# Kernel optimization log

Measured on AMD Instinct MI355X. Metric: run time of the kernel, lower is better.

## Reference

```python
import jax, jax.numpy as jnp
import numpy as np

INF = 1.0e12
V, EMB, H, H2 = 50000, 300, 512, 1024
EDGE, EEMB = 4, 32
B, TS, TQ = 16, 400, 33
MAX_OOV = 100
EXT = V + MAX_OOV
COV_HYPER = 1.0


def gru_cell(x, h, Wi, Wh, bi, bh):
    # torch GRU cell, gate order r,z,n
    gx = x @ Wi.T + bi
    gh = h @ Wh.T + bh
    hd = h.shape[-1]
    r = jax.nn.sigmoid(gx[:, :hd] + gh[:, :hd])
    z = jax.nn.sigmoid(gx[:, hd:2 * hd] + gh[:, hd:2 * hd])
    n = jnp.tanh(gx[:, 2 * hd:] + r * gh[:, 2 * hd:])
    return (1.0 - z) * n + z * h


def gru_scan(xs, h0, Wi, Wh, bi, bh, reverse=False):
    def step(h, x):
        hn = gru_cell(x, h, Wi, Wh, bi, bh)
        return hn, hn
    return jax.lax.scan(step, h0, xs, reverse=reverse)


def setup_inputs() -> dict:
    key = jax.random.key(0)
    ks = iter(jax.random.split(key, 64))
    def rp(*shape):
        return jax.random.normal(next(ks), shape, jnp.float32) * 0.05
    d = {}
    d['enc_emb'] = rp(V, EMB); d['ans_emb'] = rp(EDGE, EEMB); d['dec_emb'] = rp(V, EMB)
    in0 = EMB + EEMB
    d['eWi0'] = rp(2, 3 * H, in0); d['eWh0'] = rp(2, 3 * H, H); d['ebi0'] = rp(2, 3 * H); d['ebh0'] = rp(2, 3 * H)
    d['eWi1'] = rp(2, 3 * H, 2 * H); d['eWh1'] = rp(2, 3 * H, H); d['ebi1'] = rp(2, 3 * H); d['ebh1'] = rp(2, 3 * H)
    d['trans_W'] = rp(H2, H2); d['trans_b'] = rp(H2)
    d['upd_W'] = rp(H2, 2 * H2); d['gate_W'] = rp(H2, 2 * H2)
    din0 = EMB + H2
    d['dWi0'] = rp(3 * H2, din0); d['dWh0'] = rp(3 * H2, H2); d['dbi0'] = rp(3 * H2); d['dbh0'] = rp(3 * H2)
    d['dWi1'] = rp(3 * H2, H2); d['dWh1'] = rp(3 * H2, H2); d['dbi1'] = rp(3 * H2); d['dbh1'] = rp(3 * H2)
    d['dtrans_W'] = rp(H2, H2); d['dtrans_b'] = rp(H2)
    d['pW1'] = rp(H2, 2 * H2); d['pb1'] = rp(H2); d['pW2'] = rp(V, H2); d['pb2'] = rp(V)
    d['input_s'] = jax.random.randint(next(ks), (B, TS), 1, V)
    ext = jax.random.randint(next(ks), (B, TS), 0, EXT)
    d['ext_src_ids'] = ext.at[0, 0].set(EXT - 1)  # pin num_oov = MAX_OOV
    d['input_q'] = jax.random.randint(next(ks), (B, TQ), 1, V)
    d['input_a'] = jax.random.randint(next(ks), (B, TS), 0, EDGE)
    d['s_pos'] = jax.random.randint(next(ks), (B, TS), 0, TS)
    return d


def reference(enc_emb, ans_emb, dec_emb,
              eWi0, eWh0, ebi0, ebh0, eWi1, eWh1, ebi1, ebh1,
              trans_W, trans_b, upd_W, gate_W,
              dWi0, dWh0, dbi0, dbh0, dWi1, dWh1, dbi1, dbh1,
              dtrans_W, dtrans_b, pW1, pb1, pW2, pb2,
              input_s, ext_src_ids, input_q, input_a, s_pos):
    mask = jnp.sign(input_s)  # [B,TS] (all ones by construction)
    # ---------------- encoder ----------------
    emb = jnp.concatenate([enc_emb[input_s], ans_emb[input_a]], -1)  # [B,TS,EMB+EEMB]
    xs = emb.transpose(1, 0, 2)  # [TS,B,*]
    h0 = jnp.zeros((B, H), emb.dtype)
    h_list = []
    for (Wi, Wh, bi, bh) in ((eWi0, eWh0, ebi0, ebh0), (eWi1, eWh1, ebi1, ebh1)):
        hf, yf = gru_scan(xs, h0, Wi[0], Wh[0], bi[0], bh[0])
        hb, yb = gru_scan(xs, h0, Wi[1], Wh[1], bi[1], bh[1], reverse=True)
        xs = jnp.concatenate([yf, yb], -1)
        h_list.append(jnp.concatenate([hf, hb], -1))  # [B,H2]
    output = xs.transpose(1, 0, 2)  # [B,TS,H2]
    memories = output @ trans_W.T + trans_b
    # gated self-attention
    energies = jnp.einsum('btd,bsd->bts', output, memories)
    energies = jnp.where(mask[:, None, :] == 0, -INF, energies)
    scores = jax.nn.softmax(energies, -1)
    ctx = jnp.einsum('bts,bsd->btd', scores, output)
    inp = jnp.concatenate([output, ctx], -1)
    f_t = jnp.tanh(inp @ upd_W.T)
    g_t = jax.nn.sigmoid(inp @ gate_W.T)
    self_out = g_t * f_t + (1.0 - g_t) * output
    # answer-sentence attention (on memories, per original code)
    ans = jnp.where(input_a[..., None] == 0, 1.0, memories)
    e = memories * ans
    e = jnp.where(mask[..., None] == 0, -INF, e)
    e = jax.nn.softmax(e, axis=1)
    enc_out = self_out + e * memories
    # ---------------- decoder ----------------
    mem_d = enc_out @ dtrans_W.T + dtrans_b  # [B,TS,H2]
    emb_q = dec_emb[input_q[:, :-1]].transpose(1, 0, 2)  # [Tt,B,EMB]
    b_idx = jnp.arange(B)[:, None]

    def step(carry, emb_t):
        h0c, h1c, ctx_c, cov = carry
        rnn_in = jnp.concatenate([emb_t, ctx_c], -1)
        h0n = gru_cell(rnn_in, h0c, dWi0, dWh0, dbi0, dbh0)
        h1n = gru_cell(h0n, h1c, dWi1, dWh1, dbi1, dbh1)
        energy = jnp.einsum('bd,btd->bt', h1n, mem_d)
        sen_e = jnp.where(mask == 0, -INF, energy)
        cov_e = sen_e * (1.0 - cov)
        attn = jax.nn.softmax(cov_e, -1)
        new_ctx = jnp.einsum('bt,btd->bd', attn, mem_d)
        cov_loss = jnp.sum(jnp.minimum(attn, cov)) / B * COV_HYPER
        new_cov = cov + attn
        hid = jnp.tanh(jnp.concatenate([h1n, new_ctx], -1) @ pW1.T + pb1)
        logits = hid @ pW2.T + pb2
        ext = jnp.concatenate([logits, jnp.zeros((B, MAX_OOV), logits.dtype)], -1)
        out = jnp.full((B, EXT), -INF, logits.dtype).at[b_idx, ext_src_ids].max(cov_e)
        out = jnp.where(out == -INF, 0.0, out)
        lg = ext + out
        lg = jnp.where(lg == 0.0, -INF, lg)
        return (h0n, h1n, new_ctx, new_cov), (lg, cov_loss)

    init = (h_list[0], h_list[1], jnp.zeros((B, H2), emb.dtype), jnp.zeros((B, TS), emb.dtype))
    _, (lgs, covl) = jax.lax.scan(step, init, emb_q)
    return lgs.transpose(1, 0, 2), jnp.sum(covl) / lgs.shape[0]


if __name__ == '__main__':
    o = reference(**setup_inputs())
    print(o[0].shape, o[1])
```

## Files before the change

### kernel.cpp

```cpp
#include <hip/hip_runtime.h>
#include <stdint.h>

#define TSN 400
#define NB 16
#define HENC 512
#define HD2 1024
#define G3E 1536
#define G3D 3072
#define EMBD 300
#define AEMB 32
#define NV 50000
#define NEXT 50100
#define NVP 50176
#define NTT 32
#define NEG_INF (-1.0e12f)

typedef __attribute__((ext_vector_type(8))) short bf16x8;
typedef __attribute__((ext_vector_type(4))) float f32x4;

__device__ __forceinline__ ushort f2bf(float f) {
  unsigned u = __float_as_uint(f);
  unsigned r = (u + 0x7fffu + ((u >> 16) & 1u)) >> 16;
  return (ushort)r;
}
__device__ __forceinline__ float bf2f(ushort h) {
  return __uint_as_float((unsigned)h << 16);
}
__device__ __forceinline__ unsigned agat_ld(const unsigned* p) {
  return __hip_atomic_load(p, __ATOMIC_RELAXED, __HIP_MEMORY_SCOPE_AGENT);
}
__device__ __forceinline__ void agat_st(unsigned* p, unsigned v) {
  __hip_atomic_store(p, v, __ATOMIC_RELAXED, __HIP_MEMORY_SCOPE_AGENT);
}
__device__ __forceinline__ unsigned long long agat_ld64(const unsigned long long* p) {
  return __hip_atomic_load(p, __ATOMIC_RELAXED, __HIP_MEMORY_SCOPE_AGENT);
}

__global__ __launch_bounds__(256) void k_embed_bf(
    const float* __restrict__ enc_emb, const float* __restrict__ ans_emb,
    const int* __restrict__ input_s, const int* __restrict__ input_a,
    ushort* __restrict__ X0)
{
  long i = (long)blockIdx.x*256 + threadIdx.x;
  if (i >= (long)TSN*NB*384) return;
  int c = (int)(i % 384);
  long r = i / 384;
  int b = (int)(r % NB);
  int t = (int)(r / NB);
  float v = 0.f;
  if (c < EMBD) v = enc_emb[(long)input_s[b*TSN + t]*EMBD + c];
  else if (c < 332) v = ans_emb[(long)input_a[b*TSN + t]*AEMB + (c - EMBD)];
  X0[i] = f2bf(v);
}

__global__ __launch_bounds__(256) void k_embq_bf(
    const float* __restrict__ dec_emb, const int* __restrict__ input_q,
    ushort* __restrict__ EQ)
{
  long i = (long)blockIdx.x*256 + threadIdx.x;
  if (i >= (long)NTT*NB*320) return;
  int c = (int)(i % 320);
  long r = i / 320;
  int b = (int)(r % NB);
  int s = (int)(r / NB);
  EQ[i] = (c < EMBD) ? f2bf(dec_emb[(long)input_q[b*33 + s]*EMBD + c]) : (ushort)0;
}

__global__ __launch_bounds__(256) void k_castw(
    const float* __restrict__ src, ushort* __restrict__ dst,
    int Nsrc, long total, int Ksrc, int Kdst, int ldsrc, int coloff)
{
  long i = (long)blockIdx.x*256 + threadIdx.x;
  if (i >= total) return;
  int k = (int)(i % Kdst);
  long n = i / Kdst;
  float v = (n < Nsrc && k < Ksrc) ? src[n*ldsrc + coloff + k] : 0.f;
  dst[i] = f2bf(v);
}

__global__ __launch_bounds__(256) void k_cast8(
    const float4* __restrict__ s, ushort* __restrict__ d, long n8)
{
  long i = (long)blockIdx.x*256 + threadIdx.x;
  if (i >= n8) return;
  float4 v0 = s[2*i], v1 = s[2*i + 1];
  union { ushort u[8]; bf16x8 h; } c;
  c.u[0] = f2bf(v0.x); c.u[1] = f2bf(v0.y); c.u[2] = f2bf(v0.z); c.u[3] = f2bf(v0.w);
  c.u[4] = f2bf(v1.x); c.u[5] = f2bf(v1.y); c.u[6] = f2bf(v1.z); c.u[7] = f2bf(v1.w);
  *(bf16x8*)&d[i*8] = c.h;
}

__global__ __launch_bounds__(256) void k_cast(
    const float* __restrict__ s, ushort* __restrict__ d, long n)
{
  long i = (long)blockIdx.x*256 + threadIdx.x;
  if (i >= n) return;
  d[i] = f2bf(s[i]);
}

__global__ __launch_bounds__(256) void k_catcopy(
    const unsigned* __restrict__ src, unsigned* __restrict__ dst)
{
  long i = (long)blockIdx.x*256 + threadIdx.x;
  if (i >= 6400l*512) return;
  long r = i >> 9;
  int c = (int)(i & 511);
  dst[(r << 10) + c] = src[i];
}

__global__ __launch_bounds__(256) void k_transpose_hh(
    const ushort* __restrict__ in, ushort* __restrict__ out)
{
  __shared__ ushort tb[32][33];
  int b = blockIdx.z;
  int r0 = blockIdx.x*32, c0 = blockIdx.y*32;
  int tx = threadIdx.x & 31, ty = threadIdx.x >> 5;
  #pragma unroll
  for (int i = 0; i < 32; i += 8) {
    int r = r0 + ty + i, c = c0 + tx;
    tb[ty+i][tx] = (r < TSN) ? in[((long)b*TSN + r)*1024 + c] : (ushort)0;
  }
  __syncthreads();
  #pragma unroll
  for (int i = 0; i < 32; i += 8) {
    int c = c0 + ty + i, r = r0 + tx;
    out[((long)b*1024 + c)*448 + r] = tb[tx][ty+i];
  }
}

__global__ __launch_bounds__(256) void k_mfma_nt(
    const ushort* __restrict__ Ab, const ushort* __restrict__ Wb,
    const float* __restrict__ bias, float* __restrict__ Cb, ushort* __restrict__ C2b,
    int M, int N, int K, int lda, int ldw, int ldc,
    long sA, long sW, long sC, long sBias, int accum, int act)
{
  __shared__ ushort As[64][72];
  __shared__ ushort Ws[64][72];
  const ushort* A = Ab + (long)blockIdx.z * sA;
  const ushort* W = Wb + (long)blockIdx.z * sW;
  float* C = Cb ? Cb + (long)blockIdx.z * sC : nullptr;
  const float* bi = bias ? bias + (long)blockIdx.z * sBias : nullptr;
  const int m0 = blockIdx.x*64, n0 = blockIdx.y*64;
  const int tid = threadIdx.x;
  const int wave = tid >> 6, lane = tid & 63;
  const int wm = wave >> 1, wn = wave & 1;
  const int lr = lane & 15, kg = lane >> 4;
  f32x4 acc[2][2] = {};
  for (int k0 = 0; k0 < K; k0 += 64) {
    __syncthreads();
    #pragma unroll
    for (int it = 0; it < 2; ++it) {
      int sidx = tid + it*256;
      int r = sidx >> 3, c = (sidx & 7)*8;
      bf16x8 av = {};
      bf16x8 wv = {};
      if (m0 + r < M) av = *(const bf16x8*)&A[(long)(m0+r)*lda + k0 + c];
      if (n0 + r < N) wv = *(const bf16x8*)&W[(long)(n0+r)*ldw + k0 + c];
      *(bf16x8*)&As[r][c] = av;
      *(bf16x8*)&Ws[r][c] = wv;
    }
    __syncthreads();
    #pragma unroll
    for (int kk = 0; kk < 2; ++kk) {
      bf16x8 af[2], bf[2];
      #pragma unroll
      for (int mt = 0; mt < 2; ++mt)
        af[mt] = *(const bf16x8*)&As[wm*32 + mt*16 + lr][kk*32 + kg*8];
      #pragma unroll
      for (int nt = 0; nt < 2; ++nt)
        bf[nt] = *(const bf16x8*)&Ws[wn*32 + nt*16 + lr][kk*32 + kg*8];
      #pragma unroll
      for (int mt = 0; mt < 2; ++mt)
        #pragma unroll
        for (int nt = 0; nt < 2; ++nt)
          acc[mt][nt] = __builtin_amdgcn_mfma_f32_16x16x32_bf16(af[mt], bf[nt], acc[mt][nt], 0, 0, 0);
    }
  }
  #pragma unroll
  for (int mt = 0; mt < 2; ++mt) {
    #pragma unroll
    for (int r = 0; r < 4; ++r) {
      int m = m0 + wm*32 + mt*16 + kg*4 + r;
      if (m >= M) continue;
      #pragma unroll
      for (int nt = 0; nt < 2; ++nt) {
        int n = n0 + wn*32 + nt*16 + lr;
        if (n >= N) continue;
        float v = acc[mt][nt][r];
        if (accum && C) v += C[(long)m*ldc + n];
        if (bi)    v += bi[n];
        if (act == 1) v = tanhf(v);
        else if (act == 2) v = 1.f/(1.f + expf(-v));
        if (C) C[(long)m*ldc + n] = v;
        if (C2b) C2b[(long)blockIdx.z*sC + (long)m*ldc + n] = f2bf(v);
      }
    }
  }
}

__global__ __launch_bounds__(256, 1) void k_scan_mfma(
    const ushort* __restrict__ GXf, const ushort* __restrict__ GXb,
    const ushort* __restrict__ Whb,
    const float* __restrict__ bh,
    ushort* __restrict__ Ybf, int bmajor,
    float* __restrict__ hfin,
    ushort* __restrict__ hpp,
    int* __restrict__ slots)
{
  const int bid = blockIdx.x;
  const int tid = threadIdx.x;
  const int wg = bid*4 + (tid >> 6);
  const int lane = tid & 63;
  const int lr = lane & 15, kg = lane >> 4;
  const int dir = wg >> 5, jt = wg & 31;
  const int j = jt*16 + lr;
  __shared__ ushort hsm[16][520];
  const ushort* Wp0 = Whb + ((long)(dir*G3E + j)        << 9) + kg*8;
  const ushort* Wp1 = Whb + ((long)(dir*G3E + 512 + j)  << 9) + kg*8;
  const ushort* Wp2 = Whb + ((long)(dir*G3E + 1024 + j) << 9) + kg*8;
  bf16x8 W0[16], W1[16], W2[16];
  #pragma unroll
  for (int i = 0; i < 16; ++i) {
    W0[i] = *(const bf16x8*)(Wp0 + i*32);
    W1[i] = *(const bf16x8*)(Wp1 + i*32);
    W2[i] = *(const bf16x8*)(Wp2 + i*32);
  }
  const float bh0 = bh[dir*G3E + j];
  const float bh1 = bh[dir*G3E + 512 + j];
  const float bh2 = bh[dir*G3E + 1024 + j];
  const ushort* GX = dir ? GXb : GXf;
  unsigned* hppu = (unsigned*)hpp;
  int* myslot = slots + dir*256 + (bid & 7)*32;
  int* dslots = slots + dir*256;
  float hreg[4] = {0.f, 0.f, 0.f, 0.f};
  float g0[4], g1[4], g2[4];
  {
    const int t0 = dir ? (TSN - 1) : 0;
    const ushort* gxp = GX + (long)t0*NB*G3E + j;
    #pragma unroll
    for (int r = 0; r < 4; ++r) {
      const ushort* g = gxp + (long)(kg*4 + r)*G3E;
      g0[r] = bf2f(g[0]); g1[r] = bf2f(g[512]); g2[r] = bf2f(g[1024]);
    }
  }
  for (int s = 0; s < TSN; ++s) {
    const int cur = s & 1;
    {
      const unsigned long long* hin =
          (const unsigned long long*)hppu + (cur*2 + dir)*2048;
      unsigned long long vqw[8];
      #pragma unroll
      for (int i = 0; i < 8; ++i) vqw[i] = agat_ld64(hin + i*256 + tid);
      #pragma unroll
      for (int i = 0; i < 8; ++i) {
        int d0 = 2*(i*256 + tid);
        *(unsigned long long*)&hsm[d0 >> 8][(d0 & 255)*2] = vqw[i];
      }
    }
    __syncthreads();
    f32x4 a0 = {}, a1 = {}, a2 = {};
    #pragma unroll
    for (int i = 0; i < 16; ++i) {
      bf16x8 hf = *(const bf16x8*)&hsm[lr][kg*8 + i*32];
      a0 = __builtin_amdgcn_mfma_f32_16x16x32_bf16(hf, W0[i], a0, 0, 0, 0);
      a1 = __builtin_amdgcn_mfma_f32_16x16x32_bf16(hf, W1[i], a1, 0, 0, 0);
      a2 = __builtin_amdgcn_mfma_f32_16x16x32_bf16(hf, W2[i], a2, 0, 0, 0);
    }
    const int t = dir ? (TSN - 1 - s) : s;
    const int obase = ((cur^1)*2 + dir)*16*512;
    float hsave[4];
    #pragma unroll
    for (int r = 0; r < 4; ++r) {
      int b = kg*4 + r;
      float rr = 1.f/(1.f + expf(-(g0[r] + a0[r] + bh0)));
      float zz = 1.f/(1.f + expf(-(g1[r] + a1[r] + bh1)));
      float nn = tanhf(g2[r] + rr*(a2[r] + bh2));
      float hn = (1.f - zz)*nn + zz*hreg[r];
      hreg[r] = hn;
      hsave[r] = hn;
      unsigned hv = f2bf(hn);
      unsigned pv = (unsigned)__shfl_xor((int)hv, 1);
      if ((lr & 1) == 0)
        agat_st(hppu + ((obase + b*512 + j) >> 1), hv | (pv << 16));
    }
    if (s + 1 < TSN) {
      asm volatile("s_waitcnt vmcnt(0)" ::: "memory");
      __syncthreads();
      if (tid == 0)
        agat_st((unsigned*)myslot, (unsigned)(s + 1));
      {
        const int tn = dir ? (TSN - 2 - s) : (s + 1);
        const ushort* gxp = GX + (long)tn*NB*G3E + j;
        #pragma unroll
        for (int r = 0; r < 4; ++r) {
          const ushort* g = gxp + (long)(kg*4 + r)*G3E;
          g0[r] = bf2f(g[0]); g1[r] = bf2f(g[512]); g2[r] = bf2f(g[1024]);
        }
      }
      #pragma unroll
      for (int r = 0; r < 4; ++r) {
        int b = kg*4 + r;
        long yi = bmajor ? ((long)b*TSN + t)*1024 + dir*512 + j
                         : ((long)t*NB + b)*1024 + dir*512 + j;
        Ybf[yi] = f2bf(hsave[r]);
      }
      if (tid < 8) {
        while ((int)agat_ld((const unsigned*)(dslots + tid*32)) < s + 1)
          __builtin_amdgcn_s_sleep(1);
      }
      __syncthreads();
    } else {
      #pragma unroll
      for (int r = 0; r < 4; ++r) {
        int b = kg*4 + r;
        long yi = bmajor ? ((long)b*TSN + t)*1024 + dir*512 + j
                         : ((long)t*NB + b)*1024 + dir*512 + j;
        Ybf[yi] = f2bf(hsave[r]);
        hfin[b*1024 + dir*512 + j] = hsave[r];
      }
    }
  }
}

__global__ __launch_bounds__(256) void k_softmax_bf(
    const float* __restrict__ E, ushort* __restrict__ S)
{
  long row = blockIdx.x;
  const float* x = E + row*TSN;
  ushort* o = S + row*448;
  int tid = threadIdx.x;
  float v0 = (tid < TSN) ? x[tid] : -INFINITY;
  float v1 = (tid + 256 < TSN) ? x[tid + 256] : -INFINITY;
  __shared__ float red[256];
  red[tid] = fmaxf(v0, v1); __syncthreads();
  for (int oo = 128; oo; oo >>= 1) { if (tid < oo) red[tid] = fmaxf(red[tid], red[tid+oo]); __syncthreads(); }
  float m = red[0]; __syncthreads();
  float e0 = (tid < TSN) ? expf(v0 - m) : 0.f;
  float e1 = (tid + 256 < TSN) ? expf(v1 - m) : 0.f;
  red[tid] = e0 + e1; __syncthreads();
  for (int oo = 128; oo; oo >>= 1) { if (tid < oo) red[tid] += red[tid+oo]; __syncthreads(); }
  float inv = 1.f/red[0];
  if (tid < 192) o[tid + 256] = (tid + 256 < TSN) ? f2bf(e1*inv) : (ushort)0;
  o[tid] = f2bf(e0*inv);
}

__global__ __launch_bounds__(256) void k_ansatt2(
    const ushort* __restrict__ memsb, const ushort* __restrict__ ftgt,
    const ushort* __restrict__ outpb,
    const int* __restrict__ input_a, ushort* __restrict__ encb)
{
  int b = blockIdx.x >> 2;
  int d = (blockIdx.x & 3)*256 + threadIdx.x;
  __shared__ int ia[TSN];
  for (int i = threadIdx.x; i < TSN; i += 256) ia[i] = input_a[b*TSN + i];
  __syncthreads();
  float m = -INFINITY;
  #pragma unroll 4
  for (int t = 0; t < TSN; ++t) {
    float v = bf2f(memsb[((long)b*TSN + t)*1024 + d]);
    float e = ia[t] ? v*v : v;
    m = fmaxf(m, e);
  }
  float ssum = 0.f;
  #pragma unroll 4
  for (int t = 0; t < TSN; ++t) {
    float v = bf2f(memsb[((long)b*TSN + t)*1024 + d]);
    float e = ia[t] ? v*v : v;
    ssum += expf(e - m);
  }
  float inv = 1.f/ssum;
  #pragma unroll 4
  for (int t = 0; t < TSN; ++t) {
    long idx = ((long)b*TSN + t)*1024 + d;
    long idx2 = ((long)b*TSN + t)*2048 + d;
    float v = bf2f(memsb[idx]);
    float e = ia[t] ? v*v : v;
    float fraw = bf2f(ftgt[idx2]);
    float graw = bf2f(ftgt[idx2 + 1024]);
    float gg = 1.f/(1.f + expf(-graw));
    float selfo = gg*tanhf(fraw) + (1.f - gg)*bf2f(outpb[idx]);
    encb[idx] = f2bf(selfo + expf(e - m)*inv*v);
  }
}

__global__ __launch_bounds__(128) void k_gru_dec(
    const ushort* __restrict__ A1, const ushort* __restrict__ W1,
    const ushort* __restrict__ A2, const ushort* __restrict__ W2,
    const float* __restrict__ gxadd, const float* __restrict__ bi,
    const float* __restrict__ bh,
    const float* __restrict__ hprev, float* __restrict__ hout,
    ushort* __restrict__ houtb, ushort* __restrict__ catb)
{
  const int wv = threadIdx.x >> 6;
  const int lane = threadIdx.x & 63;
  const int lr = lane & 15, kg = lane >> 4;
  const int j = blockIdx.x*16 + lr;
  const int kb = wv*512;
  __shared__ float psum[6][16][16];
  const ushort* w1p0 = W1 + ((long)(j)        << 10) + kb + kg*8;
  const ushort* w1p1 = W1 + ((long)(1024 + j) << 10) + kb + kg*8;
  const ushort* w1p2 = W1 + ((long)(2048 + j) << 10) + kb + kg*8;
  const ushort* w2p0 = W2 + ((long)(j)        << 10) + kb + kg*8;
  const ushort* w2p1 = W2 + ((long)(1024 + j) << 10) + kb + kg*8;
  const ushort* w2p2 = W2 + ((long)(2048 + j) << 10) + kb + kg*8;
  const ushort* a1p = A1 + lr*1024 + kb + kg*8;
  const ushort* a2p = A2 + lr*1024 + kb + kg*8;
  f32x4 x0 = {}, x1 = {}, x2 = {}, h0 = {}, h1 = {}, h2 = {};
  #pragma unroll 4
  for (int k0 = 0; k0 < 512; k0 += 32) {
    bf16x8 a1v = *(const bf16x8*)(a1p + k0);
    bf16x8 a2v = *(const bf16x8*)(a2p + k0);
    x0 = __builtin_amdgcn_mfma_f32_16x16x32_bf16(a1v, *(const bf16x8*)(w1p0 + k0), x0, 0, 0, 0);
    x1 = __builtin_amdgcn_mfma_f32_16x16x32_bf16(a1v, *(const bf16x8*)(w1p1 + k0), x1, 0, 0, 0);
    x2 = __builtin_amdgcn_mfma_f32_16x16x32_bf16(a1v, *(const bf16x8*)(w1p2 + k0), x2, 0, 0, 0);
    h0 = __builtin_amdgcn_mfma_f32_16x16x32_bf16(a2v, *(const bf16x8*)(w2p0 + k0), h0, 0, 0, 0);
    h1 = __builtin_amdgcn_mfma_f32_16x16x32_bf16(a2v, *(const bf16x8*)(w2p1 + k0), h1, 0, 0, 0);
    h2 = __builtin_amdgcn_mfma_f32_16x16x32_bf16(a2v, *(const bf16x8*)(w2p2 + k0), h2, 0, 0, 0);
  }
  if (wv == 1) {
    #pragma unroll
    for (int r = 0; r < 4; ++r) {
      int b = kg*4 + r;
      psum[0][b][lr] = x0[r]; psum[1][b][lr] = x1[r]; psum[2][b][lr] = x2[r];
      psum[3][b][lr] = h0[r]; psum[4][b][lr] = h1[r]; psum[5][b][lr] = h2[r];
    }
  }
  __syncthreads();
  if (wv == 0) {
    float bi0 = bi ? bi[j] : 0.f, bi1 = bi ? bi[1024 + j] : 0.f, bi2 = bi ? bi[2048 + j] : 0.f;
    float bh0 = bh[j], bh1 = bh[1024 + j], bh2 = bh[2048 + j];
    #pragma unroll
    for (int r = 0; r < 4; ++r) {
      int b = kg*4 + r;
      float gxa0 = gxadd ? gxadd[(long)b*G3D + j]        : 0.f;
      float gxa1 = gxadd ? gxadd[(long)b*G3D + 1024 + j] : 0.f;
      float gxa2 = gxadd ? gxadd[(long)b*G3D + 2048 + j] : 0.f;
      float gx0 = x0[r] + psum[0][b][lr] + gxa0 + bi0;
      float gx1 = x1[r] + psum[1][b][lr] + gxa1 + bi1;
      float gx2 = x2[r] + psum[2][b][lr] + gxa2 + bi2;
      float gh0 = h0[r] + psum[3][b][lr] + bh0;
      float gh1 = h1[r] + psum[4][b][lr] + bh1;
      float gh2 = h2[r] + psum[5][b][lr] + bh2;
      float rr = 1.f/(1.f + expf(-(gx0 + gh0)));
      float zz = 1.f/(1.f + expf(-(gx1 + gh1)));
      float nn = tanhf(gx2 + rr*gh2);
      float hp = hprev[b*1024 + j];
      float hn = (1.f - zz)*nn + zz*hp;
      hout[b*1024 + j] = hn;
      houtb[b*1024 + j] = f2bf(hn);
      if (catb) catb[(long)b*2048 + j] = f2bf(hn);
    }
  }
}

__global__ __launch_bounds__(256) void k_dec_attn3(
    const ushort* __restrict__ h1b, const ushort* __restrict__ memdb,
    float* __restrict__ cov, float* __restrict__ coveS, float* __restrict__ covacc,
    float* __restrict__ scb,
    ushort* __restrict__ ctxn, ushort* __restrict__ catb,
    int* __restrict__ slots, int epoch)
{
  const int bid = blockIdx.x, tid = threadIdx.x;
  const int b = bid >> 2, q = bid & 3;
  const int wv = tid >> 6, lane = tid & 63;
  __shared__ float at[TSN];
  __shared__ float red[256];
  __shared__ float psD[4][64][4];
  float hr[16];
  {
    bf16x8 hv0 = *(const bf16x8*)&h1b[b*1024 + lane*16];
    bf16x8 hv1 = *(const bf16x8*)&h1b[b*1024 + lane*16 + 8];
    #pragma unroll
    for (int e = 0; e < 8; ++e) { hr[e] = bf2f((ushort)hv0[e]); hr[8+e] = bf2f((ushort)hv1[e]); }
  }
  #pragma unroll 2
  for (int i = 0; i < 25; ++i) {
    int t = q*100 + wv*25 + i;
    const ushort* row = memdb + ((long)b*TSN + t)*1024 + lane*16;
    bf16x8 r0 = *(const bf16x8*)row;
    bf16x8 r1 = *(const bf16x8*)(row + 8);
    float p = 0.f;
    #pragma unroll
    for (int e = 0; e < 8; ++e) p += hr[e]*bf2f((ushort)r0[e]) + hr[8+e]*bf2f((ushort)r1[e]);
    #pragma unroll
    for (int off = 32; off; off >>= 1) p += __shfl_xor(p, off);
    if (lane == 0) agat_st((unsigned*)&scb[b*TSN + t], __float_as_uint(p));
  }
  asm volatile("s_waitcnt vmcnt(0)" ::: "memory");
  __syncthreads();
  if (tid == 0) agat_st((unsigned*)(slots + bid*32), (unsigned)epoch);
  if (tid < 64) {
    while ((int)agat_ld((const unsigned*)(slots + tid*32)) < epoch)
      __builtin_amdgcn_s_sleep(1);
  }
  __syncthreads();
  {
    bool t1v = tid < 144;
    float sc0 = __uint_as_float(agat_ld((const unsigned*)&scb[b*TSN + tid]));
    float sc1 = t1v ? __uint_as_float(agat_ld((const unsigned*)&scb[b*TSN + 256 + tid])) : 0.f;
    float co0 = cov[b*TSN + tid];
    float co1 = t1v ? cov[b*TSN + 256 + tid] : 0.f;
    float ce0 = sc0*(1.f - co0);
    float ce1 = t1v ? sc1*(1.f - co1) : -INFINITY;
// ... 160 lines not shown
  }
}

__global__ void k_covout(const float* __restrict__ covacc, float* __restrict__ outp)
{
  outp[(long)NB*NTT*NEXT] = covacc[0] * (1.0f/(NB*NTT));
}

extern "C" void kernel_launch(void* const* d_in, const int* in_sizes, int n_in,
                              void* d_out, int out_size, void* d_ws, size_t ws_size,
                              hipStream_t stream) {
  (void)in_sizes; (void)n_in; (void)out_size; (void)ws_size;
  const float* enc_emb = (const float*)d_in[0];
  const float* ans_emb = (const float*)d_in[1];
  const float* dec_emb = (const float*)d_in[2];
  const float* eWi0 = (const float*)d_in[3];
  const float* eWh0 = (const float*)d_in[4];
  const float* ebi0 = (const float*)d_in[5];
  const float* ebh0 = (const float*)d_in[6];
  const float* eWi1 = (const float*)d_in[7];
  const float* eWh1 = (const float*)d_in[8];
  const float* ebi1 = (const float*)d_in[9];
  const float* ebh1 = (const float*)d_in[10];
  const float* trans_W = (const float*)d_in[11];
  const float* trans_b = (const float*)d_in[12];
  const float* upd_W = (const float*)d_in[13];
  const float* gate_W = (const float*)d_in[14];
  const float* dWi0 = (const float*)d_in[15];
  const float* dWh0 = (const float*)d_in[16];
  const float* dbi0 = (const float*)d_in[17];
  const float* dbh0 = (const float*)d_in[18];
  const float* dWi1 = (const float*)d_in[19];
  const float* dWh1 = (const float*)d_in[20];
  const float* dbi1 = (const float*)d_in[21];
  const float* dbh1 = (const float*)d_in[22];
  const float* dtrans_W = (const float*)d_in[23];
  const float* dtrans_b = (const float*)d_in[24];
  const float* pW1 = (const float*)d_in[25];
  const float* pb1 = (const float*)d_in[26];
  const float* pW2 = (const float*)d_in[27];
  const float* pb2 = (const float*)d_in[28];
  const int* input_s = (const int*)d_in[29];
  const int* ext_ids = (const int*)d_in[30];
  const int* input_q = (const int*)d_in[31];
  const int* input_a = (const int*)d_in[32];
  float* out = (float*)d_out;

  float* ws = (float*)d_ws;
  size_t off = 0;
  auto alloc = [&](size_t n) { float* p = ws + off; off += (n + 15) & ~(size_t)15; return p; };
  auto alloch = [&](size_t nh) { return (ushort*)alloc((nh + 1) / 2); };

  ushort* hpp  = alloch(2ull*2*NB*HENC);
  int*   bar   = (int*)alloc(4096);
  float* covacc= alloc(4);
  float* cov   = alloc(NB*TSN);
  float* scb   = alloc(NB*TSN);
  unsigned* ubuf = (unsigned*)alloc((size_t)NB*NEXT);
  float* hfin0 = alloc(NB*HD2);
  float* hfin1 = alloc(NB*HD2);
  float* dh0   = alloc(2ull*NB*HD2);
  float* dh1   = alloc(2ull*NB*HD2);
  ushort* h0b  = alloch(2ull*NB*HD2);
  ushort* h1b  = alloch(2ull*NB*HD2);
  ushort* ctxbf= alloch(2ull*NB*HD2);
  ushort* catbf= alloch((size_t)NB*2048);
  ushort* hidAll = alloch((size_t)NTT*NB*HD2);
  float* coveAll = alloc((size_t)NTT*NB*TSN);

  ushort* eWi0c   = alloch(2ull*G3E*384);
  ushort* eWi1c   = alloch(2ull*G3E*1024);
  ushort* Whb0    = alloch(2ull*G3E*HENC);
  ushort* Whb1    = alloch(2ull*G3E*HENC);
  ushort* transWb = alloch(1024ull*1024);
  ushort* fgWb    = alloch(2048ull*2048);
  ushort* dtransWb= alloch(1024ull*1024);
  ushort* dWi0e   = alloch(3072ull*320);
  ushort* dWi0c   = alloch(3072ull*1024);
  ushort* dWh0b   = alloch(3072ull*1024);
  ushort* dWi1b   = alloch(3072ull*1024);
  ushort* dWh1b   = alloch(3072ull*1024);
  ushort* pW1b    = alloch(1024ull*2048);

  size_t regionStart = off;
  float*  GXr  = alloc(2ull*6400*G3E);
  ushort* GXbf = (ushort*)GXr;
  ushort* X0c  = alloch(6400ull*384);
  ushort* Y0bf = alloch(6400ull*1024);
  alloc(6400ull*HD2);
  ushort* ftgt_bf = (ushort*)(ws + regionStart);
  ushort* pW2b    = (ushort*)(ws + regionStart);
  ushort* outpTb  = (ushort*)(ws + regionStart + 26000000);

  ushort* outpbf = alloch(6400ull*HD2);
  ushort* memsbf = alloch(6400ull*HD2);
  ushort* catE   = alloch(6400ull*2048);
  float*  energ  = alloc((size_t)NB*TSN*TSN);
  ushort* scoresb= alloch((size_t)NB*TSN*448);
  ushort* memd_bf= alloch(6400ull*HD2);
  ushort* encbf  = alloch(6400ull*HD2);
  ushort* embqb  = alloch(512ull*320);
  float*  embGX  = alloc(512ull*G3D);

  k_embed_bf<<<9600, 256, 0, stream>>>(enc_emb, ans_emb, input_s, input_a, X0c);
  k_castw<<<4608, 256, 0, stream>>>(eWi0, eWi0c, 3072, 3072ull*384, 332, 384, 332, 0);
  k_cast8<<<1536, 256, 0, stream>>>((const float4*)eWi1, eWi1c, 393216);
  k_cast8<<<768, 256, 0, stream>>>((const float4*)eWh0, Whb0, 196608);
  k_cast8<<<768, 256, 0, stream>>>((const float4*)eWh1, Whb1, 196608);
  k_cast8<<<512, 256, 0, stream>>>((const float4*)trans_W, transWb, 131072);
  k_cast8<<<1024, 256, 0, stream>>>((const float4*)upd_W,  fgWb, 262144);
  k_cast8<<<1024, 256, 0, stream>>>((const float4*)gate_W, fgWb + 1024ull*2048, 262144);
  k_cast8<<<512, 256, 0, stream>>>((const float4*)dtrans_W, dtransWb, 131072);
  k_castw<<<3840, 256, 0, stream>>>(dWi0, dWi0e, 3072, 3072ull*320, 300, 320, 1324, 0);
  k_castw<<<12288, 256, 0, stream>>>(dWi0, dWi0c, 3072, 3072ull*1024, 1024, 1024, 1324, 300);
  k_cast8<<<1536, 256, 0, stream>>>((const float4*)dWh0, dWh0b, 393216);
  k_cast8<<<1536, 256, 0, stream>>>((const float4*)dWi1, dWi1b, 393216);
  k_cast8<<<1536, 256, 0, stream>>>((const float4*)dWh1, dWh1b, 393216);
  k_cast8<<<1024, 256, 0, stream>>>((const float4*)pW1, pW1b, 262144);

  hipMemsetAsync(bar, 0, 16384, stream);

  k_mfma_nt<<<dim3(100,24,2), 256, 0, stream>>>(X0c, eWi0c, ebi0, nullptr, GXbf,
      6400, G3E, 384, 384, 384, G3E, 0, (long)G3E*384, 6400ull*G3E, G3E, 0, 0);
  hipMemsetAsync(hpp, 0, 2ull*2*NB*HENC*2, stream);
  k_scan_mfma<<<16, 256, 0, stream>>>(GXbf, GXbf + 6400ull*G3E, Whb0, ebh0,
      Y0bf, 0, hfin0, hpp, bar);
  k_mfma_nt<<<dim3(100,24,2), 256, 0, stream>>>(Y0bf, eWi1c, ebi1, nullptr, GXbf,
      6400, G3E, 1024, 1024, 1024, G3E, 0, (long)G3E*1024, 6400ull*G3E, G3E, 0, 0);
  hipMemsetAsync(hpp, 0, 2ull*2*NB*HENC*2, stream);
  k_scan_mfma<<<16, 256, 0, stream>>>(GXbf, GXbf + 6400ull*G3E, Whb1, ebh1,
      outpbf, 1, hfin1, hpp, bar + 512);

  k_mfma_nt<<<dim3(100,16,1), 256, 0, stream>>>(outpbf, transWb, trans_b, nullptr, memsbf,
      6400, HD2, 1024, 1024, 1024, HD2, 0, 0, 0, 0, 0, 0);
  k_mfma_nt<<<dim3(7,7,16), 256, 0, stream>>>(outpbf, memsbf, nullptr, energ, nullptr,
      TSN, TSN, 1024, 1024, 1024, TSN, (long)TSN*1024, (long)TSN*1024, (long)TSN*TSN, 0, 0, 0);
  k_softmax_bf<<<NB*TSN, 256, 0, stream>>>(energ, scoresb);
  k_transpose_hh<<<dim3(14,32,16), 256, 0, stream>>>(outpbf, outpTb);
  k_mfma_nt<<<dim3(7,16,16), 256, 0, stream>>>(scoresb, outpTb, nullptr, nullptr, catE + 1024,
      TSN, HD2, 448, 448, 448, 2048, (long)TSN*448, (long)HD2*448, (long)TSN*2048, 0, 0, 0);
  k_catcopy<<<12800, 256, 0, stream>>>((const unsigned*)outpbf, (unsigned*)catE);
  k_mfma_nt<<<dim3(100,32,1), 256, 0, stream>>>(catE, fgWb, nullptr, nullptr, ftgt_bf,
      6400, 2048, 2048, 2048, 2048, 2048, 0, 0, 0, 0, 0, 0);
  k_ansatt2<<<64, 256, 0, stream>>>(memsbf, ftgt_bf, outpbf, input_a, encbf);
  k_cast8<<<25000, 256, 0, stream>>>((const float4*)pW2, pW2b, 6400000);
  hipMemsetAsync(pW2b + 50000l*1024, 0, 176l*1024*2, stream);
  k_mfma_nt<<<dim3(100,16,1), 256, 0, stream>>>(encbf, dtransWb, dtrans_b, nullptr, memd_bf,
      6400, HD2, 1024, 1024, 1024, HD2, 0, 0, 0, 0, 0, 0);

  k_embq_bf<<<640, 256, 0, stream>>>(dec_emb, input_q, embqb);
  k_mfma_nt<<<dim3(8,48,1), 256, 0, stream>>>(embqb, dWi0e, dbi0, embGX, nullptr,
      NTT*NB, G3D, 320, 320, 320, G3D, 0, 0, 0, 0, 0, 0);

  hipMemsetAsync(cov, 0, (size_t)NB*TSN*4, stream);
  hipMemsetAsync(covacc, 0, 4, stream);
  hipMemsetAsync(ubuf, 0, (size_t)NB*NEXT*4, stream);
  hipMemsetAsync(ctxbf, 0, (size_t)NB*HD2*2, stream);
  hipMemcpyAsync(dh0, hfin0, (size_t)NB*HD2*4, hipMemcpyDeviceToDevice, stream);
  hipMemcpyAsync(dh1, hfin1, (size_t)NB*HD2*4, hipMemcpyDeviceToDevice, stream);
  k_cast<<<64, 256, 0, stream>>>(hfin0, h0b, 16384);
  k_cast<<<64, 256, 0, stream>>>(hfin1, h1b, 16384);

  for (int s = 0; s < NTT; ++s) {
    int cur = s & 1, nxt = cur ^ 1;
    float* h0c = dh0 + (size_t)cur*NB*HD2;  float* h0n = dh0 + (size_t)nxt*NB*HD2;
    float* h1c = dh1 + (size_t)cur*NB*HD2;  float* h1n = dh1 + (size_t)nxt*NB*HD2;
    ushort* h0bc = h0b + (size_t)cur*NB*HD2; ushort* h0bn = h0b + (size_t)nxt*NB*HD2;
    ushort* h1bc = h1b + (size_t)cur*NB*HD2; ushort* h1bn = h1b + (size_t)nxt*NB*HD2;
    ushort* ctxc = ctxbf + (size_t)cur*NB*HD2; ushort* ctxn = ctxbf + (size_t)nxt*NB*HD2;

    k_gru_dec<<<64, 128, 0, stream>>>(ctxc, dWi0c, h0bc, dWh0b,
        embGX + (size_t)s*NB*G3D, nullptr, dbh0, h0c, h0n, h0bn, nullptr);
    k_gru_dec<<<64, 128, 0, stream>>>(h0bn, dWi1b, h1bc, dWh1b,
        nullptr, dbi1, dbh1, h1c, h1n, h1bn, catbf);
    k_dec_attn3<<<64, 256, 0, stream>>>(h1bn, memd_bf,
        cov, coveAll + (size_t)s*NB*TSN, covacc, scb, ctxn, catbf,
        bar + 1024, s + 1);
    k_hid<<<64, 128, 0, stream>>>(catbf, pW1b, pb1, hidAll + (size_t)s*NB*HD2);
  }
  k_logits_all<<<dim3(196, 4), 256, 0, stream>>>(hidAll, pW2b, pb2, out);
  k_compose_all<<<NB, 512, 0, stream>>>(ext_ids, coveAll, ubuf, out);
  k_covout<<<1, 1, 0, stream>>>(covacc, out);
}
```

Measured before the change: 6.017 ms.

## Fuse decoder GRU layers, overlap weight casts with scan, write scan output into concat buffer

```diff
diff --git a/kernel.cpp b/kernel.cpp
--- a/kernel.cpp
+++ b/kernel.cpp
@@ -18,6 +18,9 @@
 typedef __attribute__((ext_vector_type(8))) short bf16x8;
 typedef __attribute__((ext_vector_type(4))) float f32x4;
 
+struct CJob { const float4* s; ushort* d; long n8; };
+struct CJobs { CJob j[10]; int nj; };
+
 __device__ __forceinline__ ushort f2bf(float f) {
   unsigned u = __float_as_uint(f);
   unsigned r = (u + 0x7fffu + ((u >> 16) & 1u)) >> 16;
@@ -98,18 +101,8 @@
   d[i] = f2bf(s[i]);
 }
 
-__global__ __launch_bounds__(256) void k_catcopy(
-    const unsigned* __restrict__ src, unsigned* __restrict__ dst)
-{
-  long i = (long)blockIdx.x*256 + threadIdx.x;
-  if (i >= 6400l*512) return;
-  long r = i >> 9;
-  int c = (int)(i & 511);
-  dst[(r << 10) + c] = src[i];
-}
-
 __global__ __launch_bounds__(256) void k_transpose_hh(
-    const ushort* __restrict__ in, ushort* __restrict__ out)
+    const ushort* __restrict__ in, ushort* __restrict__ out, int ldin)
 {
   __shared__ ushort tb[32][33];
   int b = blockIdx.z;
@@ -118,7 +111,7 @@
   #pragma unroll
   for (int i = 0; i < 32; i += 8) {
     int r = r0 + ty + i, c = c0 + tx;
-    tb[ty+i][tx] = (r < TSN) ? in[((long)b*TSN + r)*1024 + c] : (ushort)0;
+    tb[ty+i][tx] = (r < TSN) ? in[((long)b*TSN + r)*ldin + c] : (ushort)0;
   }
   __syncthreads();
   #pragma unroll
@@ -202,13 +195,31 @@
     const ushort* __restrict__ GXf, const ushort* __restrict__ GXb,
     const ushort* __restrict__ Whb,
     const float* __restrict__ bh,
-    ushort* __restrict__ Ybf, int bmajor,
+    ushort* __restrict__ Ybf, int bmajor, int ldY,
     float* __restrict__ hfin,
     ushort* __restrict__ hpp,
-    int* __restrict__ slots)
+    int* __restrict__ slots,
+    CJobs jobs, int nScan)
 {
   const int bid = blockIdx.x;
   const int tid = threadIdx.x;
+  if (bid >= nScan) {
+    const int eb = bid - nScan;
+    const long nE = (long)(gridDim.x - nScan)*256;
+    for (int ji = 0; ji < jobs.nj; ++ji) {
+      const float4* s = jobs.j[ji].s;
+      ushort* d = jobs.j[ji].d;
+      const long n8 = jobs.j[ji].n8;
+      for (long i = (long)eb*256 + tid; i < n8; i += nE) {
+        float4 v0 = s[2*i], v1 = s[2*i + 1];
+        union { ushort u[8]; bf16x8 h; } c;
+        c.u[0] = f2bf(v0.x); c.u[1] = f2bf(v0.y); c.u[2] = f2bf(v0.z); c.u[3] = f2bf(v0.w);
+        c.u[4] = f2bf(v1.x); c.u[5] = f2bf(v1.y); c.u[6] = f2bf(v1.z); c.u[7] = f2bf(v1.w);
+        *(bf16x8*)&d[i*8] = c.h;
+      }
+    }
+    return;
+  }
   const int wg = bid*4 + (tid >> 6);
   const int lane = tid & 63;
   const int lr = lane & 15, kg = lane >> 4;
@@ -300,7 +311,7 @@
       #pragma unroll
       for (int r = 0; r < 4; ++r) {
         int b = kg*4 + r;
-        long yi = bmajor ? ((long)b*TSN + t)*1024 + dir*512 + j
+        long yi = bmajor ? ((long)b*TSN + t)*ldY + dir*512 + j
                          : ((long)t*NB + b)*1024 + dir*512 + j;
         Ybf[yi] = f2bf(hsave[r]);
       }
@@ -313,7 +324,7 @@
       #pragma unroll
       for (int r = 0; r < 4; ++r) {
         int b = kg*4 + r;
-        long yi = bmajor ? ((long)b*TSN + t)*1024 + dir*512 + j
+        long yi = bmajor ? ((long)b*TSN + t)*ldY + dir*512 + j
                          : ((long)t*NB + b)*1024 + dir*512 + j;
         Ybf[yi] = f2bf(hsave[r]);
         hfin[b*1024 + dir*512 + j] = hsave[r];
@@ -378,77 +389,159 @@
     float fraw = bf2f(ftgt[idx2]);
     float graw = bf2f(ftgt[idx2 + 1024]);
     float gg = 1.f/(1.f + expf(-graw));
-    float selfo = gg*tanhf(fraw) + (1.f - gg)*bf2f(outpb[idx]);
+    float selfo = gg*tanhf(fraw) + (1.f - gg)*bf2f(outpb[idx2]);
     encb[idx] = f2bf(selfo + expf(e - m)*inv*v);
   }
 }
 
-__global__ __launch_bounds__(128) void k_gru_dec(
-    const ushort* __restrict__ A1, const ushort* __restrict__ W1,
-    const ushort* __restrict__ A2, const ushort* __restrict__ W2,
-    const float* __restrict__ gxadd, const float* __restrict__ bi,
-    const float* __restrict__ bh,
-    const float* __restrict__ hprev, float* __restrict__ hout,
-    ushort* __restrict__ houtb, ushort* __restrict__ catb)
-{
-  const int wv = threadIdx.x >> 6;
-  const int lane = threadIdx.x & 63;
+__global__ __launch_bounds__(128) void k_gru2(
+    const ushort* __restrict__ ctxc, const ushort* __restrict__ Wi0,
+    const ushort* __restrict__ h0bc, const ushort* __restrict__ Wh0,
+    const float* __restrict__ gx0add, const float* __restrict__ bh0v,
+    const float* __restrict__ h0prev, float* __restrict__ h0out, ushort* __restrict__ h0bn,
+    const ushort* __restrict__ Wi1,
+    const ushort* __restrict__ h1bc, const ushort* __restrict__ Wh1,
+    const float* __restrict__ bi1, const float* __restrict__ bh1v,
+    const float* __restrict__ h1prev, float* __restrict__ h1out, ushort* __restrict__ h1bn,
+    ushort* __restrict__ catb,
+    int* __restrict__ slots, int epoch)
+{
+  const int tid = threadIdx.x;
+  const int wv = tid >> 6;
+  const int lane = tid & 63;
   const int lr = lane & 15, kg = lane >> 4;
-  const int j = blockIdx.x*16 + lr;
+  const int bid = blockIdx.x;
+  const int j = bid*16 + lr;
   const int kb = wv*512;
   __shared__ float psum[6][16][16];
-  const ushort* w1p0 = W1 + ((long)(j)        << 10) + kb + kg*8;
-  const ushort* w1p1 = W1 + ((long)(1024 + j) << 10) + kb + kg*8;
-  const ushort* w1p2 = W1 + ((long)(2048 + j) << 10) + kb + kg*8;
-  const ushort* w2p0 = W2 + ((long)(j)        << 10) + kb + kg*8;
-  const ushort* w2p1 = W2 + ((long)(1024 + j) << 10) + kb + kg*8;
-  const ushort* w2p2 = W2 + ((long)(2048 + j) << 10) + kb + kg*8;
-  const ushort* a1p = A1 + lr*1024 + kb + kg*8;
-  const ushort* a2p = A2 + lr*1024 + kb + kg*8;
-  f32x4 x0 = {}, x1 = {}, x2 = {}, h0 = {}, h1 = {}, h2 = {};
-  #pragma unroll 4
-  for (int k0 = 0; k0 < 512; k0 += 32) {
-    bf16x8 a1v = *(const bf16x8*)(a1p + k0);
-    bf16x8 a2v = *(const bf16x8*)(a2p + k0);
-    x0 = __builtin_amdgcn_mfma_f32_16x16x32_bf16(a1v, *(const bf16x8*)(w1p0 + k0), x0, 0, 0, 0);
-    x1 = __builtin_amdgcn_mfma_f32_16x16x32_bf16(a1v, *(const bf16x8*)(w1p1 + k0), x1, 0, 0, 0);
-    x2 = __builtin_amdgcn_mfma_f32_16x16x32_bf16(a1v, *(const bf16x8*)(w1p2 + k0), x2, 0, 0, 0);
-    h0 = __builtin_amdgcn_mfma_f32_16x16x32_bf16(a2v, *(const bf16x8*)(w2p0 + k0), h0, 0, 0, 0);
-    h1 = __builtin_amdgcn_mfma_f32_16x16x32_bf16(a2v, *(const bf16x8*)(w2p1 + k0), h1, 0, 0, 0);
-    h2 = __builtin_amdgcn_mfma_f32_16x16x32_bf16(a2v, *(const bf16x8*)(w2p2 + k0), h2, 0, 0, 0);
-  }
-  if (wv == 1) {
-    #pragma unroll
-    for (int r = 0; r < 4; ++r) {
-      int b = kg*4 + r;
-      psum[0][b][lr] = x0[r]; psum[1][b][lr] = x1[r]; psum[2][b][lr] = x2[r];
-      psum[3][b][lr] = h0[r]; psum[4][b][lr] = h1[r]; psum[5][b][lr] = h2[r];
-    }
-  }
+  __shared__ ushort hsm[2][16][520];
+  {
+    const ushort* a1p = ctxc + lr*1024 + kb + kg*8;
+    const ushort* a2p = h0bc + lr*1024 + kb + kg*8;
+    const long wro = (long)j*1024 + kb + kg*8;
+    const ushort* w10 = Wi0 + wro;
+    const ushort* w11 = Wi0 + wro + 1024l*1024;
+    const ushort* w12 = Wi0 + wro + 2048l*1024;
+    const ushort* w20 = Wh0 + wro;
+    const ushort* w21 = Wh0 + wro + 1024l*1024;
+    const ushort* w22 = Wh0 + wro + 2048l*1024;
+    f32x4 x0 = {}, x1 = {}, x2 = {}, h0a = {}, h1a = {}, h2a = {};
+    #pragma unroll 4
+    for (int k0 = 0; k0 < 512; k0 += 32) {
+      bf16x8 a1v = *(const bf16x8*)(a1p + k0);
+      bf16x8 a2v = *(const bf16x8*)(a2p + k0);
+      x0 = __builtin_amdgcn_mfma_f32_16x16x32_bf16(a1v, *(const bf16x8*)(w10 + k0), x0, 0, 0, 0);
+      x1 = __builtin_amdgcn_mfma_f32_16x16x32_bf16(a1v, *(const bf16x8*)(w11 + k0), x1, 0, 0, 0);
+      x2 = __builtin_amdgcn_mfma_f32_16x16x32_bf16(a1v, *(const bf16x8*)(w12 + k0), x2, 0, 0, 0);
+      h0a = __builtin_amdgcn_mfma_f32_16x16x32_bf16(a2v, *(const bf16x8*)(w20 + k0), h0a, 0, 0, 0);
+      h1a = __builtin_amdgcn_mfma_f32_16x16x32_bf16(a2v, *(const bf16x8*)(w21 + k0), h1a, 0, 0, 0);
+      h2a = __builtin_amdgcn_mfma_f32_16x16x32_bf16(a2v, *(const bf16x8*)(w22 + k0), h2a, 0, 0, 0);
+    }
+    if (wv == 1) {
+      #pragma unroll
+      for (int r = 0; r < 4; ++r) {
+        int b = kg*4 + r;
+        psum[0][b][lr] = x0[r]; psum[1][b][lr] = x1[r]; psum[2][b][lr] = x2[r];
+        psum[3][b][lr] = h0a[r]; psum[4][b][lr] = h1a[r]; psum[5][b][lr] = h2a[r];
+      }
+    }
+    __syncthreads();
+    if (wv == 0) {
+      float bh0 = bh0v[j], bh1 = bh0v[1024 + j], bh2 = bh0v[2048 + j];
+      #pragma unroll
+      for (int r = 0; r < 4; ++r) {
+        int b = kg*4 + r;
+        const float* g = gx0add + (long)b*G3D;
+        float gx0 = x0[r] + psum[0][b][lr] + g[j];
+        float gx1 = x1[r] + psum[1][b][lr] + g[1024 + j];
+        float gx2 = x2[r] + psum[2][b][lr] + g[2048 + j];
+        float gh0 = h0a[r] + psum[3][b][lr] + bh0;
+        float gh1 = h1a[r] + psum[4][b][lr] + bh1;
+        float gh2 = h2a[r] + psum[5][b][lr] + bh2;
+        float rr = 1.f/(1.f + expf(-(gx0 + gh0)));
+        float zz = 1.f/(1.f + expf(-(gx1 + gh1)));
+        float nn = tanhf(gx2 + rr*gh2);
+        float hp = h0prev[b*1024 + j];
+        float hn = (1.f - zz)*nn + zz*hp;
+        h0out[b*1024 + j] = hn;
+        unsigned hv = f2bf(hn);
+        unsigned pv = (unsigned)__shfl_xor((int)hv, 1);
+        if ((lr & 1) == 0)
+          agat_st((unsigned*)h0bn + ((b*1024 + j) >> 1), hv | (pv << 16));
+      }
+    }
+  }
+  asm volatile("s_waitcnt vmcnt(0)" ::: "memory");
   __syncthreads();
-  if (wv == 0) {
-    float bi0 = bi ? bi[j] : 0.f, bi1 = bi ? bi[1024 + j] : 0.f, bi2 = bi ? bi[2048 + j] : 0.f;
-    float bh0 = bh[j], bh1 = bh[1024 + j], bh2 = bh[2048 + j];
-    #pragma unroll
-    for (int r = 0; r < 4; ++r) {
-      int b = kg*4 + r;
-      float gxa0 = gxadd ? gxadd[(long)b*G3D + j]        : 0.f;
-      float gxa1 = gxadd ? gxadd[(long)b*G3D + 1024 + j] : 0.f;
-      float gxa2 = gxadd ? gxadd[(long)b*G3D + 2048 + j] : 0.f;
-      float gx0 = x0[r] + psum[0][b][lr] + gxa0 + bi0;
-      float gx1 = x1[r] + psum[1][b][lr] + gxa1 + bi1;
-      float gx2 = x2[r] + psum[2][b][lr] + gxa2 + bi2;
-      float gh0 = h0[r] + psum[3][b][lr] + bh0;
-      float gh1 = h1[r] + psum[4][b][lr] + bh1;
-      float gh2 = h2[r] + psum[5][b][lr] + bh2;
-      float rr = 1.f/(1.f + expf(-(gx0 + gh0)));
-      float zz = 1.f/(1.f + expf(-(gx1 + gh1)));
-      float nn = tanhf(gx2 + rr*gh2);
-      float hp = hprev[b*1024 + j];
-      float hn = (1.f - zz)*nn + zz*hp;
-      hout[b*1024 + j] = hn;
-      houtb[b*1024 + j] = f2bf(hn);
-      if (catb) catb[(long)b*2048 + j] = f2bf(hn);
+  if (tid == 0) agat_st((unsigned*)(slots + bid*32), (unsigned)epoch);
+  if (tid < 64) {
+    while ((int)agat_ld((const unsigned*)(slots + tid*32)) < epoch)
+      __builtin_amdgcn_s_sleep(1);
+  }
+  __syncthreads();
+  {
+    const unsigned long long* src = (const unsigned long long*)h0bn;
+    #pragma unroll
+    for (int i = 0; i < 32; ++i) {
+      int idx = i*64 + lane;
+      int row = idx >> 7, cq = idx & 127;
+      unsigned long long v = agat_ld64(src + row*256 + (kb >> 2) + cq);
+      *(unsigned long long*)&hsm[wv][row][cq*4] = v;
+    }
+  }
+  __syncthreads();
+  {
+    const ushort* a2p = h1bc + lr*1024 + kb + kg*8;
+    const long wro = (long)j*1024 + kb + kg*8;
+    const ushort* w10 = Wi1 + wro;
+    const ushort* w11 = Wi1 + wro + 1024l*1024;
+    const ushort* w12 = Wi1 + wro + 2048l*1024;
+    const ushort* w20 = Wh1 + wro;
+    const ushort* w21 = Wh1 + wro + 1024l*1024;
+    const ushort* w22 = Wh1 + wro + 2048l*1024;
+    f32x4 x0 = {}, x1 = {}, x2 = {}, h0a = {}, h1a = {}, h2a = {};
+    #pragma unroll 4
+    for (int k0 = 0; k0 < 512; k0 += 32) {
+      bf16x8 a1v = *(const bf16x8*)&hsm[wv][lr][kg*8 + k0];
+      bf16x8 a2v = *(const bf16x8*)(a2p + k0);
+      x0 = __builtin_amdgcn_mfma_f32_16x16x32_bf16(a1v, *(const bf16x8*)(w10 + k0), x0, 0, 0, 0);
+      x1 = __builtin_amdgcn_mfma_f32_16x16x32_bf16(a1v, *(const bf16x8*)(w11 + k0), x1, 0, 0, 0);
+      x2 = __builtin_amdgcn_mfma_f32_16x16x32_bf16(a1v, *(const bf16x8*)(w12 + k0), x2, 0, 0, 0);
+      h0a = __builtin_amdgcn_mfma_f32_16x16x32_bf16(a2v, *(const bf16x8*)(w20 + k0), h0a, 0, 0, 0);
+      h1a = __builtin_amdgcn_mfma_f32_16x16x32_bf16(a2v, *(const bf16x8*)(w21 + k0), h1a, 0, 0, 0);
+      h2a = __builtin_amdgcn_mfma_f32_16x16x32_bf16(a2v, *(const bf16x8*)(w22 + k0), h2a, 0, 0, 0);
+    }
+    __syncthreads();
+    if (wv == 1) {
+      #pragma unroll
+      for (int r = 0; r < 4; ++r) {
+        int b = kg*4 + r;
+        psum[0][b][lr] = x0[r]; psum[1][b][lr] = x1[r]; psum[2][b][lr] = x2[r];
+        psum[3][b][lr] = h0a[r]; psum[4][b][lr] = h1a[r]; psum[5][b][lr] = h2a[r];
+      }
+    }
+    __syncthreads();
+    if (wv == 0) {
+      float bi0 = bi1[j], bi1v = bi1[1024 + j], bi2 = bi1[2048 + j];
+      float bh0 = bh1v[j], bh1 = bh1v[1024 + j], bh2 = bh1v[2048 + j];
+      #pragma unroll
+      for (int r = 0; r < 4; ++r) {
+        int b = kg*4 + r;
+        float gx0 = x0[r] + psum[0][b][lr] + bi0;
+        float gx1 = x1[r] + psum[1][b][lr] + bi1v;
+        float gx2 = x2[r] + psum[2][b][lr] + bi2;
+        float gh0 = h0a[r] + psum[3][b][lr] + bh0;
+        float gh1 = h1a[r] + psum[4][b][lr] + bh1;
+        float gh2 = h2a[r] + psum[5][b][lr] + bh2;
+        float rr = 1.f/(1.f + expf(-(gx0 + gh0)));
+        float zz = 1.f/(1.f + expf(-(gx1 + gh1)));
+        float nn = tanhf(gx2 + rr*gh2);
+        float hp = h1prev[b*1024 + j];
+        float hn = (1.f - zz)*nn + zz*hp;
+        h1out[b*1024 + j] = hn;
+        h1bn[b*1024 + j] = f2bf(hn);
+        catb[(long)b*2048 + j] = f2bf(hn);
+      }
     }
   }
 }
@@ -715,7 +808,7 @@
   auto alloch = [&](size_t nh) { return (ushort*)alloc((nh + 1) / 2); };
 
   ushort* hpp  = alloch(2ull*2*NB*HENC);
-  int*   bar   = (int*)alloc(4096);
+  int*   bar   = (int*)alloc(8192);
   float* covacc= alloc(4);
   float* cov   = alloc(NB*TSN);
   float* scb   = alloc(NB*TSN);
@@ -755,7 +848,6 @@
   ushort* pW2b    = (ushort*)(ws + regionStart);
   ushort* outpTb  = (ushort*)(ws + regionStart + 26000000);
 
-  ushort* outpbf = alloch(6400ull*HD2);
   ushort* memsbf = alloch(6400ull*HD2);
   ushort* catE   = alloch(6400ull*2048);
   float*  energ  = alloc((size_t)NB*TSN*TSN);
@@ -767,45 +859,51 @@
 
   k_embed_bf<<<9600, 256, 0, stream>>>(enc_emb, ans_emb, input_s, input_a, X0c);
   k_castw<<<4608, 256, 0, stream>>>(eWi0, eWi0c, 3072, 3072ull*384, 332, 384, 332, 0);
-  k_cast8<<<1536, 256, 0, stream>>>((const float4*)eWi1, eWi1c, 393216);
   k_cast8<<<768, 256, 0, stream>>>((const float4*)eWh0, Whb0, 196608);
-  k_cast8<<<768, 256, 0, stream>>>((const float4*)eWh1, Whb1, 196608);
-  k_cast8<<<512, 256, 0, stream>>>((const float4*)trans_W, transWb, 131072);
-  k_cast8<<<1024, 256, 0, stream>>>((const float4*)upd_W,  fgWb, 262144);
-  k_cast8<<<1024, 256, 0, stream>>>((const float4*)gate_W, fgWb + 1024ull*2048, 262144);
-  k_cast8<<<512, 256, 0, stream>>>((const float4*)dtrans_W, dtransWb, 131072);
   k_castw<<<3840, 256, 0, stream>>>(dWi0, dWi0e, 3072, 3072ull*320, 300, 320, 1324, 0);
   k_castw<<<12288, 256, 0, stream>>>(dWi0, dWi0c, 3072, 3072ull*1024, 1024, 1024, 1324, 300);
-  k_cast8<<<1536, 256, 0, stream>>>((const float4*)dWh0, dWh0b, 393216);
-  k_cast8<<<1536, 256, 0, stream>>>((const float4*)dWi1, dWi1b, 393216);
-  k_cast8<<<1536, 256, 0, stream>>>((const float4*)dWh1, dWh1b, 393216);
-  k_cast8<<<1024, 256, 0, stream>>>((const float4*)pW1, pW1b, 262144);
-
-  hipMemsetAsync(bar, 0, 16384, stream);
+
+  hipMemsetAsync(bar, 0, 32768, stream);
 
   k_mfma_nt<<<dim3(100,24,2), 256, 0, stream>>>(X0c, eWi0c, ebi0, nullptr, GXbf,
       6400, G3E, 384, 384, 384, G3E, 0, (long)G3E*384, 6400ull*G3E, G3E, 0, 0);
   hipMemsetAsync(hpp, 0, 2ull*2*NB*HENC*2, stream);
-  k_scan_mfma<<<16, 256, 0, stream>>>(GXbf, GXbf + 6400ull*G3E, Whb0, ebh0,
-      Y0bf, 0, hfin0, hpp, bar);
+  {
+    CJobs jobs;
+    jobs.nj = 10;
+    jobs.j[0] = { (const float4*)eWi1,   eWi1c,              393216 };
+    jobs.j[1] = { (const float4*)eWh1,   Whb1,               196608 };
+    jobs.j[2] = { (const float4*)trans_W, transWb,           131072 };
+    jobs.j[3] = { (const float4*)upd_W,  fgWb,               262144 };
+    jobs.j[4] = { (const float4*)gate_W, fgWb + 1024ull*2048, 262144 };
+    jobs.j[5] = { (const float4*)dtrans_W, dtransWb,         131072 };
+    jobs.j[6] = { (const float4*)dWh0,   dWh0b,              393216 };
+    jobs.j[7] = { (const float4*)dWi1,   dWi1b,              393216 };
+    jobs.j[8] = { (const float4*)dWh1,   dWh1b,              393216 };
+    jobs.j[9] = { (const float4*)pW1,    pW1b,               262144 };
+    k_scan_mfma<<<208, 256, 0, stream>>>(GXbf, GXbf + 6400ull*G3E, Whb0, ebh0,
+        Y0bf, 0, 1024, hfin0, hpp, bar, jobs, 16);
+  }
   k_mfma_nt<<<dim3(100,24,2), 256, 0, stream>>>(Y0bf, eWi1c, ebi1, nullptr, GXbf,
       6400, G3E, 1024, 1024, 1024, G3E, 0, (long)G3E*1024, 6400ull*G3E, G3E, 0, 0);
   hipMemsetAsync(hpp, 0, 2ull*2*NB*HENC*2, stream);
-  k_scan_mfma<<<16, 256, 0, stream>>>(GXbf, GXbf + 6400ull*G3E, Whb1, ebh1,
-      outpbf, 1, hfin1, hpp, bar + 512);
-
-  k_mfma_nt<<<dim3(100,16,1), 256, 0, stream>>>(outpbf, transWb, trans_b, nullptr, memsbf,
-      6400, HD2, 1024, 1024, 1024, HD2, 0, 0, 0, 0, 0, 0);
-  k_mfma_nt<<<dim3(7,7,16), 256, 0, stream>>>(outpbf, memsbf, nullptr, energ, nullptr,
-      TSN, TSN, 1024, 1024, 1024, TSN, (long)TSN*1024, (long)TSN*1024, (long)TSN*TSN, 0, 0, 0);
+  {
+    CJobs none; none.nj = 0;
+    k_scan_mfma<<<16, 256, 0, stream>>>(GXbf, GXbf + 6400ull*G3E, Whb1, ebh1,
+        catE, 1, 2048, hfin1, hpp, bar + 512, none, 16);
+  }
+
+  k_mfma_nt<<<dim3(100,16,1), 256, 0, stream>>>(catE, transWb, trans_b, nullptr, memsbf,
+      6400, HD2, 1024, 2048, 1024, HD2, 0, 0, 0, 0, 0, 0);
+  k_mfma_nt<<<dim3(7,7,16), 256, 0, stream>>>(catE, memsbf, nullptr, energ, nullptr,
+      TSN, TSN, 1024, 2048, 1024, TSN, (long)TSN*2048, (long)TSN*1024, (long)TSN*TSN, 0, 0, 0);
   k_softmax_bf<<<NB*TSN, 256, 0, stream>>>(energ, scoresb);
-  k_transpose_hh<<<dim3(14,32,16), 256, 0, stream>>>(outpbf, outpTb);
+  k_transpose_hh<<<dim3(14,32,16), 256, 0, stream>>>(catE, outpTb, 2048);
   k_mfma_nt<<<dim3(7,16,16), 256, 0, stream>>>(scoresb, outpTb, nullptr, nullptr, catE + 1024,
       TSN, HD2, 448, 448, 448, 2048, (long)TSN*448, (long)HD2*448, (long)TSN*2048, 0, 0, 0);
-  k_catcopy<<<12800, 256, 0, stream>>>((const unsigned*)outpbf, (unsigned*)catE);
   k_mfma_nt<<<dim3(100,32,1), 256, 0, stream>>>(catE, fgWb, nullptr, nullptr, ftgt_bf,
       6400, 2048, 2048, 2048, 2048, 2048, 0, 0, 0, 0, 0, 0);
-  k_ansatt2<<<64, 256, 0, stream>>>(memsbf, ftgt_bf, outpbf, input_a, encbf);
+  k_ansatt2<<<64, 256, 0, stream>>>(memsbf, ftgt_bf, catE, input_a, encbf);
   k_cast8<<<25000, 256, 0, stream>>>((const float4*)pW2, pW2b, 6400000);
   hipMemsetAsync(pW2b + 50000l*1024, 0, 176l*1024*2, stream);
   k_mfma_nt<<<dim3(100,16,1), 256, 0, stream>>>(encbf, dtransWb, dtrans_b, nullptr, memd_bf,
@@ -832,10 +930,10 @@
     ushort* h1bc = h1b + (size_t)cur*NB*HD2; ushort* h1bn = h1b + (size_t)nxt*NB*HD2;
     ushort* ctxc = ctxbf + (size_t)cur*NB*HD2; ushort* ctxn = ctxbf + (size_t)nxt*NB*HD2;
 
-    k_gru_dec<<<64, 128, 0, stream>>>(ctxc, dWi0c, h0bc, dWh0b,
-        embGX + (size_t)s*NB*G3D, nullptr, dbh0, h0c, h0n, h0bn, nullptr);
-    k_gru_dec<<<64, 128, 0, stream>>>(h0bn, dWi1b, h1bc, dWh1b,
-        nullptr, dbi1, dbh1, h1c, h1n, h1bn, catbf);
+    k_gru2<<<64, 128, 0, stream>>>(ctxc, dWi0c, h0bc, dWh0b,
+        embGX + (size_t)s*NB*G3D, dbh0, h0c, h0n, h0bn,
+        dWi1b, h1bc, dWh1b, dbi1, dbh1, h1c, h1n, h1bn, catbf,
+        bar + 3072, s + 1);
     k_dec_attn3<<<64, 256, 0, stream>>>(h1bn, memd_bf,
         cov, coveAll + (size_t)s*NB*TSN, covacc, scb, ctxn, catbf,
         bar + 1024, s + 1);
```

New measurement: 6.521 ms. 8.4% more time.
